# Performance work log

Measured on AMD Instinct MI355X. Metric: run time of the kernel, lower is better.

Reference implementation:

```python
import jax, jax.numpy as jnp
import numpy as np

N_NODES = 50000
NEG_SLOPE = 0.2


def _gat_conv(x, src, dst, W, a_src, a_dst, b, num_nodes):
    # W: [H*C, F_in]; a_src/a_dst: [H, C]; b: [H*C]
    H, C = a_src.shape
    xp = (x @ W.T).reshape(num_nodes, H, C)              # [N,H,C]
    alpha_s = jnp.sum(xp * a_src[None], axis=-1)          # [N,H]
    alpha_d = jnp.sum(xp * a_dst[None], axis=-1)          # [N,H]
    e = jax.nn.leaky_relu(alpha_s[src] + alpha_d[dst], NEG_SLOPE)  # [E,H]
    # segment softmax over incoming edges of each dst node (self-loops guarantee non-empty segments)
    m = jax.ops.segment_max(e, dst, num_segments=num_nodes)
    e = jnp.exp(e - m[dst])
    s = jax.ops.segment_sum(e, dst, num_segments=num_nodes)
    alpha = e / s[dst]                                    # [E,H]
    out = jax.ops.segment_sum(alpha[:, :, None] * xp[src], dst, num_segments=num_nodes)  # [N,H,C]
    return out.reshape(num_nodes, H * C) + b


def setup_inputs() -> dict:
    key = jax.random.key(0)
    ks = jax.random.split(key, 12)
    N, E, F_in, HID, H, Z = N_NODES, 800000, 128, 64, 2, 32
    sc = 0.1
    return {
        "features": jax.random.normal(ks[0], (N, F_in), jnp.float32),
        "edges": jax.random.randint(ks[1], (2, E), 0, N, jnp.int32),
        "W1": jax.random.normal(ks[2], (H * HID, F_in), jnp.float32) * sc,
        "a_src1": jax.random.normal(ks[3], (H, HID), jnp.float32) * sc,
        "a_dst1": jax.random.normal(ks[4], (H, HID), jnp.float32) * sc,
        "b1": jnp.zeros((H * HID,), jnp.float32),
        "W_mu": jax.random.normal(ks[5], (Z, H * HID), jnp.float32) * sc,
        "a_src_mu": jax.random.normal(ks[6], (1, Z), jnp.float32) * sc,
        "a_dst_mu": jax.random.normal(ks[7], (1, Z), jnp.float32) * sc,
        "b_mu": jnp.zeros((Z,), jnp.float32),
        "W_std": jax.random.normal(ks[8], (Z, H * HID), jnp.float32) * sc,
        "a_src_std": jax.random.normal(ks[9], (1, Z), jnp.float32) * sc,
        "a_dst_std": jax.random.normal(ks[10], (1, Z), jnp.float32) * sc,
        "b_std": jnp.zeros((Z,), jnp.float32),
    }


def reference(features, edges, W1, a_src1, a_dst1, b1, W_mu, a_src_mu, a_dst_mu, b_mu, W_std, a_src_std, a_dst_std, b_std):
    N = features.shape[0]
    loops = jnp.arange(N, dtype=edges.dtype)
    src = jnp.concatenate([edges[0], loops])  # add self loops (PyG default)
    dst = jnp.concatenate([edges[1], loops])
    h = _gat_conv(features, src, dst, W1, a_src1, a_dst1, b1, N)
    h = jax.nn.relu(h)  # dropout p=0.0 -> identity
    mu = _gat_conv(h, src, dst, W_mu, a_src_mu, a_dst_mu, b_mu, N)
    std = _gat_conv(h, src, dst, W_std, a_src_std, a_dst_std, b_std, N)
    return (mu, std)
```

## Files before the change

### kernel.cpp

```cpp
#include <hip/hip_runtime.h>
#include <math.h>

#define N_NODES 50000
#define N_EDGES 800000
#define ET (N_EDGES + N_NODES)
#define KD 128
#define Z 32
#define SH 7
#define BW 128
#define NBUCK ((N_NODES + BW - 1) / BW)
#define CHUNK 2048
#define NBLKA ((ET + CHUNK - 1) / CHUNK)
#define MTOT (NBUCK * NBLKA)
#define MBS ((MTOT + 1023) / 1024)

typedef __attribute__((ext_vector_type(8))) short bf16x8;
typedef __attribute__((ext_vector_type(4))) float f32x4;

static __device__ __forceinline__ float lrelu(float x){ return x > 0.f ? x : 0.2f*x; }
static __device__ __forceinline__ float bf2f(unsigned int u16){ return __uint_as_float(u16 << 16); }
static __device__ __forceinline__ unsigned short f2bf(float f){
  unsigned int x = __float_as_uint(f);
  return (unsigned short)((x + 0x7fffu + ((x >> 16) & 1u)) >> 16);
}

__global__ __launch_bounds__(256) void bhistA_kernel(const int* __restrict__ edges, int* __restrict__ M){
  int k = blockIdx.x, t = threadIdx.x;
  __shared__ int cnt[NBUCK];
  for(int b = t; b < NBUCK; b += 256) cnt[b] = 0;
  __syncthreads();
  int base = k*CHUNK;
  int lim = min(base + CHUNK, ET);
  for(int i = base + t; i < lim; i += 256){
    int d = (i < N_EDGES) ? edges[N_EDGES + i] : (i - N_EDGES);
    atomicAdd(&cnt[d >> SH], 1);
  }
  __syncthreads();
  for(int b = t; b < NBUCK; b += 256) M[b*NBLKA + k] = cnt[b];
}

__global__ __launch_bounds__(256) void scanM1_kernel(const int* __restrict__ M, int* __restrict__ bsumM){
  int b = blockIdx.x, t = threadIdx.x;
  int base = b*1024 + t*4;
  int s = 0;
  #pragma unroll
  for(int i=0;i<4;i++){ int n = base+i; if(n < MTOT) s += M[n]; }
  for(int off=32; off; off>>=1) s += __shfl_xor(s, off);
  __shared__ int ws[4];
  if((t&63)==0) ws[t>>6] = s;
  __syncthreads();
  if(t==0) bsumM[b] = ws[0]+ws[1]+ws[2]+ws[3];
}

__global__ __launch_bounds__(256) void scanM2_kernel(const int* __restrict__ bsumM, int* __restrict__ bpreM){
  __shared__ int sm[256];
  int t = threadIdx.x;
  int v = (t < MBS) ? bsumM[t] : 0;
  sm[t] = v;
  __syncthreads();
  for(int off=1; off<256; off<<=1){
    int u = (t >= off) ? sm[t-off] : 0;
    __syncthreads();
    sm[t] += u;
    __syncthreads();
  }
  if(t < MBS) bpreM[t] = sm[t] - v;
}

__global__ __launch_bounds__(256) void scanM3_kernel(const int* __restrict__ M, const int* __restrict__ bpreM,
                                                     int* __restrict__ Mpos){
  int b = blockIdx.x, t = threadIdx.x;
  int lane = t & 63, wv = t >> 6;
  int base = b*1024 + t*4;
  int d[4]; int s = 0;
  #pragma unroll
  for(int i=0;i<4;i++){ int n = base+i; d[i] = (n < MTOT) ? M[n] : 0; s += d[i]; }
  int v = s;
  for(int off=1; off<64; off<<=1){
    int u = __shfl_up(v, off);
    if(lane >= off) v += u;
  }
  int texcl = v - s;
  __shared__ int wtot[4];
  if(lane == 63) wtot[wv] = v;
  __syncthreads();
  int woff = 0;
  for(int i=0;i<wv;i++) woff += wtot[i];
  int run = bpreM[b] + woff + texcl;
  #pragma unroll
  for(int i=0;i<4;i++){
    int n = base+i;
    if(n < MTOT){ Mpos[n] = run; run += d[i]; }
  }
}

__global__ __launch_bounds__(256) void bplaceA_kernel(const int* __restrict__ edges, const int* __restrict__ Mpos,
                                                      int2* __restrict__ etmp){
  int k = blockIdx.x, t = threadIdx.x;
  __shared__ int cur[NBUCK];
  for(int b = t; b < NBUCK; b += 256) cur[b] = Mpos[b*NBLKA + k];
  __syncthreads();
  int base = k*CHUNK;
  int lim = min(base + CHUNK, ET);
  for(int i = base + t; i < lim; i += 256){
    int s, d;
    if(i < N_EDGES){ s = edges[i]; d = edges[N_EDGES+i]; } else { s = d = i - N_EDGES; }
    int pos = atomicAdd(&cur[d >> SH], 1);
    etmp[pos] = make_int2(s, d);
  }
}

__global__ __launch_bounds__(256) void bfin_kernel(const int* __restrict__ Mpos, const int2* __restrict__ etmp,
                                                   int* __restrict__ rowptr, int2* __restrict__ epair){
  int b = blockIdx.x, t = threadIdx.x;
  __shared__ int cnt[BW];
  __shared__ int pre[BW];
  __shared__ int lcur[BW];
  if(t < BW) cnt[t] = 0;
  __syncthreads();
  int beg = Mpos[b*NBLKA];
  int end = (b+1 < NBUCK) ? Mpos[(b+1)*NBLKA] : ET;
  for(int i = beg + t; i < end; i += 256) atomicAdd(&cnt[etmp[i].y & (BW-1)], 1);
  __syncthreads();
  if(t < BW) pre[t] = cnt[t];
  __syncthreads();
  for(int off=1; off<BW; off<<=1){
    int u = 0;
    if(t < BW && t >= off) u = pre[t-off];
    __syncthreads();
    if(t < BW) pre[t] += u;
    __syncthreads();
  }
  if(t < BW){
    int excl = pre[t] - cnt[t];
    int node = b*BW + t;
    if(node < N_NODES) rowptr[node] = beg + excl;
    lcur[t] = beg + excl;
  }
  if(b == 0 && t == 255) rowptr[N_NODES] = ET;
  __syncthreads();
  for(int i = beg + t; i < end; i += 256){
    int2 e = etmp[i];
    int pos = atomicAdd(&lcur[e.y & (BW-1)], 1);
    epair[pos] = e;
  }
}

__global__ __launch_bounds__(256) void wconv_kernel(const float* __restrict__ W1,
                                                    const float* __restrict__ Wmu, const float* __restrict__ Wst,
                                                    unsigned short* __restrict__ Wb1, unsigned short* __restrict__ Wb2){
  int i = blockIdx.x*256 + threadIdx.x;
  if(i < 128*KD) Wb1[i] = f2bf(W1[i]);
  if(i < 64*KD) Wb2[i] = f2bf(i < 32*KD ? Wmu[i] : Wst[i - 32*KD]);
}

__global__ __launch_bounds__(256) void mmt1_kernel(const float* __restrict__ X,
                                                   const unsigned short* __restrict__ Wb,
                                                   const float* __restrict__ asv, const float* __restrict__ adv,
                                                   unsigned short* __restrict__ outb,
                                                   float* __restrict__ as1, float* __restrict__ ad1){
  constexpr int OC = 128, CT = 8;
  int t = threadIdx.x;
  int w = t >> 6, L = t & 63;
  int col = L & 15, quad = L >> 4;
  int row0 = blockIdx.x*64 + w*16;
  int rA = row0 + col;
  if(rA >= N_NODES) rA = N_NODES-1;

  f32x4 acc[CT];
  #pragma unroll
  for(int ct=0;ct<CT;ct++) acc[ct] = (f32x4){0.f,0.f,0.f,0.f};

  #pragma unroll
  for(int kc=0;kc<4;kc++){
    int k0 = kc*32 + quad*8;
    const float* Xf = X + (size_t)rA*KD + k0;
    float4 p = *(const float4*)Xf;
    float4 q = *(const float4*)(Xf + 4);
    bf16x8 a;
    a[0] = (short)f2bf(p.x); a[1] = (short)f2bf(p.y);
    a[2] = (short)f2bf(p.z); a[3] = (short)f2bf(p.w);
    a[4] = (short)f2bf(q.x); a[5] = (short)f2bf(q.y);
    a[6] = (short)f2bf(q.z); a[7] = (short)f2bf(q.w);
    #pragma unroll
    for(int ct=0;ct<CT;ct++){
      bf16x8 b = *(const bf16x8*)(Wb + (size_t)(ct*16 + col)*KD + k0);
      acc[ct] = __builtin_amdgcn_mfma_f32_16x16x32_bf16(a, b, acc[ct], 0, 0, 0);
    }
  }

  float av[CT], dv[CT];
  #pragma unroll
  for(int ct=0;ct<CT;ct++){ av[ct] = asv[ct*16 + col]; dv[ct] = adv[ct*16 + col]; }

  #pragma unroll
  for(int r=0;r<4;r++){
    int row = row0 + quad*4 + r;
    #pragma unroll
    for(int ct=0;ct<CT;ct++)
      if(row < N_NODES) outb[(size_t)row*OC + ct*16 + col] = f2bf(acc[ct][r]);
    float s0 = acc[0][r]*av[0] + acc[1][r]*av[1] + acc[2][r]*av[2] + acc[3][r]*av[3];
    float s1 = acc[4][r]*av[4] + acc[5][r]*av[5] + acc[6][r]*av[6] + acc[7][r]*av[7];
    float d0 = acc[0][r]*dv[0] + acc[1][r]*dv[1] + acc[2][r]*dv[2] + acc[3][r]*dv[3];
    float d1 = acc[4][r]*dv[4] + acc[5][r]*dv[5] + acc[6][r]*dv[6] + acc[7][r]*dv[7];
    #pragma unroll
    for(int off=1; off<16; off<<=1){
      s0 += __shfl_xor(s0, off); s1 += __shfl_xor(s1, off);
      d0 += __shfl_xor(d0, off); d1 += __shfl_xor(d1, off);
    }
    if(col == 0 && row < N_NODES){
      as1[row*2] = s0; as1[row*2+1] = s1;
      ad1[row*2] = d0; ad1[row*2+1] = d1;
    }
  }
}

__global__ __launch_bounds__(256) void mmt2_kernel(const unsigned short* __restrict__ Xb,
                                                   const unsigned short* __restrict__ Wb,
                                                   const float* __restrict__ asmu, const float* __restrict__ admu,
                                                   const float* __restrict__ asst, const float* __restrict__ adst,
                                                   unsigned short* __restrict__ outb,
                                                   float* __restrict__ as2, float* __restrict__ ad2){
  constexpr int OC = 64, CT = 4;
  int t = threadIdx.x;
  int w = t >> 6, L = t & 63;
  int col = L & 15, quad = L >> 4;
  int row0 = blockIdx.x*64 + w*16;
  int rA = row0 + col;
  if(rA >= N_NODES) rA = N_NODES-1;

  f32x4 acc[CT];
  #pragma unroll
  for(int ct=0;ct<CT;ct++) acc[ct] = (f32x4){0.f,0.f,0.f,0.f};

  #pragma unroll
  for(int kc=0;kc<4;kc++){
    int k0 = kc*32 + quad*8;
    bf16x8 a = *(const bf16x8*)(Xb + (size_t)rA*KD + k0);
    #pragma unroll
    for(int ct=0;ct<CT;ct++){
      bf16x8 b = *(const bf16x8*)(Wb + (size_t)(ct*16 + col)*KD + k0);
      acc[ct] = __builtin_amdgcn_mfma_f32_16x16x32_bf16(a, b, acc[ct], 0, 0, 0);
    }
  }

  float av[CT], dv[CT];
  #pragma unroll
  for(int ct=0;ct<CT;ct++){
    av[ct] = (ct < 2) ? asmu[ct*16 + col] : asst[(ct-2)*16 + col];
    dv[ct] = (ct < 2) ? admu[ct*16 + col] : adst[(ct-2)*16 + col];
  }

  #pragma unroll
  for(int r=0;r<4;r++){
    int row = row0 + quad*4 + r;
    #pragma unroll
    for(int ct=0;ct<CT;ct++)
      if(row < N_NODES) outb[(size_t)row*OC + ct*16 + col] = f2bf(acc[ct][r]);
    float smu = acc[0][r]*av[0] + acc[1][r]*av[1];
    float sst = acc[2][r]*av[2] + acc[3][r]*av[3];
    float dmu = acc[0][r]*dv[0] + acc[1][r]*dv[1];
    float dst = acc[2][r]*dv[2] + acc[3][r]*dv[3];
    #pragma unroll
    for(int off=1; off<16; off<<=1){
      smu += __shfl_xor(smu, off); sst += __shfl_xor(sst, off);
      dmu += __shfl_xor(dmu, off); dst += __shfl_xor(dst, off);
    }
    if(col == 0 && row < N_NODES){
      as2[row*2] = smu; as2[row*2+1] = sst;
      ad2[row*2] = dmu; ad2[row*2+1] = dst;
    }
  }
}

__global__ __launch_bounds__(256) void wcalc_kernel(const int2* __restrict__ epair,
                                                    const float* __restrict__ asv, const float* __restrict__ adv,
                                                    float2* __restrict__ wbuf){
  int i = blockIdx.x*256 + threadIdx.x;
  if(i >= ET) return;
  int2 e = epair[i];
  float2 a = ((const float2*)asv)[e.x];
  float2 b = ((const float2*)adv)[e.y];
  float2 w;
  w.x = __expf(lrelu(a.x + b.x));
  w.y = __expf(lrelu(a.y + b.y));
  wbuf[i] = w;
}

__global__ __launch_bounds__(256) void agg1_kernel(const int* __restrict__ rowptr, const int2* __restrict__ epair,
                                                   const float2* __restrict__ wbuf, const unsigned int* __restrict__ xb,
                                                   const float* __restrict__ b1, unsigned int* __restrict__ hb){
  int node = blockIdx.x*4 + (threadIdx.x>>6);
  int l = threadIdx.x & 63;
  if(node >= N_NODES) return;
  int beg = rowptr[node], end = rowptr[node+1];
  float accx = 0.f, accy = 0.f, s0 = 0.f, s1 = 0.f;
  int n = end - beg;
  int nq = n & ~7;
  for(int q = 0; q < nq; q += 8){
    int e0 = epair[beg+q+0].x, e1 = epair[beg+q+1].x, e2 = epair[beg+q+2].x, e3 = epair[beg+q+3].x;
    int e4 = epair[beg+q+4].x, e5 = epair[beg+q+5].x, e6 = epair[beg+q+6].x, e7 = epair[beg+q+7].x;
    float2 w0 = wbuf[beg+q+0], w1 = wbuf[beg+q+1], w2 = wbuf[beg+q+2], w3 = wbuf[beg+q+3];
    float2 w4 = wbuf[beg+q+4], w5 = wbuf[beg+q+5], w6 = wbuf[beg+q+6], w7 = wbuf[beg+q+7];
    unsigned int u0 = xb[(size_t)e0*64 + l], u1 = xb[(size_t)e1*64 + l];
    unsigned int u2 = xb[(size_t)e2*64 + l], u3 = xb[(size_t)e3*64 + l];
    unsigned int u4 = xb[(size_t)e4*64 + l], u5 = xb[(size_t)e5*64 + l];
    unsigned int u6 = xb[(size_t)e6*64 + l], u7 = xb[(size_t)e7*64 + l];
    s0 += w0.x + w1.x + w2.x + w3.x + w4.x + w5.x + w6.x + w7.x;
    s1 += w0.y + w1.y + w2.y + w3.y + w4.y + w5.y + w6.y + w7.y;
    float v0 = (l < 32) ? w0.x : w0.y;
    float v1 = (l < 32) ? w1.x : w1.y;
    float v2 = (l < 32) ? w2.x : w2.y;
    float v3 = (l < 32) ? w3.x : w3.y;
    float v4 = (l < 32) ? w4.x : w4.y;
    float v5 = (l < 32) ? w5.x : w5.y;
    float v6 = (l < 32) ? w6.x : w6.y;
    float v7 = (l < 32) ? w7.x : w7.y;
    accx += v0*__uint_as_float(u0<<16) + v1*__uint_as_float(u1<<16)
          + v2*__uint_as_float(u2<<16) + v3*__uint_as_float(u3<<16)
          + v4*__uint_as_float(u4<<16) + v5*__uint_as_float(u5<<16)
          + v6*__uint_as_float(u6<<16) + v7*__uint_as_float(u7<<16);
    accy += v0*__uint_as_float(u0&0xffff0000u) + v1*__uint_as_float(u1&0xffff0000u)
          + v2*__uint_as_float(u2&0xffff0000u) + v3*__uint_as_float(u3&0xffff0000u)
          + v4*__uint_as_float(u4&0xffff0000u) + v5*__uint_as_float(u5&0xffff0000u)
          + v6*__uint_as_float(u6&0xffff0000u) + v7*__uint_as_float(u7&0xffff0000u);
  }
  for(int i = beg + nq; i < end; i++){
    int s = epair[i].x;
    float2 w = wbuf[i];
    s0 += w.x; s1 += w.y;
    unsigned int u = xb[(size_t)s*64 + l];
    float ww = (l < 32) ? w.x : w.y;
    accx += ww * __uint_as_float(u<<16);
    accy += ww * __uint_as_float(u&0xffff0000u);
  }
  float sd = (l < 32) ? s0 : s1;
  float2 bb = ((const float2*)b1)[l];
  float rx = fmaxf(accx/sd + bb.x, 0.f);
  float ry = fmaxf(accy/sd + bb.y, 0.f);
  unsigned int hp = (unsigned int)f2bf(rx) | ((unsigned int)f2bf(ry) << 16);
  hb[(size_t)node*64 + l] = hp;
}

__global__ __launch_bounds__(256) void agg2_kernel(const int* __restrict__ rowptr, const int2* __restrict__ epair,
                                                   const float2* __restrict__ wbuf, const unsigned short* __restrict__ xb2,
                                                   const float* __restrict__ bmu, const float* __restrict__ bst,
                                                   float* __restrict__ out){
  int node = blockIdx.x*4 + (threadIdx.x>>6);
  int l = threadIdx.x & 63;
  if(node >= N_NODES) return;
  int half = l >> 5, c = l & 31;
  int beg = rowptr[node], end = rowptr[node+1];
  float acc = 0.f, ssum = 0.f;
  int n = end - beg;
  int nq = n & ~7;
  for(int q = 0; q < nq; q += 8){
    int e0 = epair[beg+q+0].x, e1 = epair[beg+q+1].x, e2 = epair[beg+q+2].x, e3 = epair[beg+q+3].x;
    int e4 = epair[beg+q+4].x, e5 = epair[beg+q+5].x, e6 = epair[beg+q+6].x, e7 = epair[beg+q+7].x;
    float2 w0 = wbuf[beg+q+0], w1 = wbuf[beg+q+1], w2 = wbuf[beg+q+2], w3 = wbuf[beg+q+3];
    float2 w4 = wbuf[beg+q+4], w5 = wbuf[beg+q+5], w6 = wbuf[beg+q+6], w7 = wbuf[beg+q+7];
    float x0 = bf2f(xb2[(size_t)e0*64 + l]), x1 = bf2f(xb2[(size_t)e1*64 + l]);
    float x2 = bf2f(xb2[(size_t)e2*64 + l]), x3 = bf2f(xb2[(size_t)e3*64 + l]);
    float x4 = bf2f(xb2[(size_t)e4*64 + l]), x5 = bf2f(xb2[(size_t)e5*64 + l]);
    float x6 = bf2f(xb2[(size_t)e6*64 + l]), x7 = bf2f(xb2[(size_t)e7*64 + l]);
    float v0 = half ? w0.y : w0.x;
    float v1 = half ? w1.y : w1.x;
    float v2 = half ? w2.y : w2.x;
    float v3 = half ? w3.y : w3.x;
    float v4 = half ? w4.y : w4.x;
    float v5 = half ? w5.y : w5.x;
    float v6 = half ? w6.y : w6.x;
    float v7 = half ? w7.y : w7.x;
    ssum += v0 + v1 + v2 + v3 + v4 + v5 + v6 + v7;
    acc  += v0*x0 + v1*x1 + v2*x2 + v3*x3 + v4*x4 + v5*x5 + v6*x6 + v7*x7;
  }
  for(int i = beg + nq; i < end; i++){
    int s = epair[i].x;
    float2 w = wbuf[i];
    float ww = half ? w.y : w.x;
    ssum += ww;
    acc += ww * bf2f(xb2[(size_t)s*64 + l]);
  }
  float r = acc/ssum + (half ? bst[c] : bmu[c]);
  out[(half ? (size_t)N_NODES*Z : 0) + (size_t)node*Z + c] = r;
}

extern "C" void kernel_launch(void* const* d_in, const int* in_sizes, int n_in,
                              void* d_out, int out_size, void* d_ws, size_t ws_size,
                              hipStream_t stream){
  const float* x    = (const float*)d_in[0];
  const int*   edges= (const int*)d_in[1];
  const float* W1   = (const float*)d_in[2];
  const float* as1v = (const float*)d_in[3];
  const float* ad1v = (const float*)d_in[4];
  const float* b1   = (const float*)d_in[5];
  const float* Wmu  = (const float*)d_in[6];
  const float* asmu = (const float*)d_in[7];
  const float* admu = (const float*)d_in[8];
  const float* bmu  = (const float*)d_in[9];
  const float* Wst  = (const float*)d_in[10];
  const float* asst = (const float*)d_in[11];
  const float* adst = (const float*)d_in[12];
  const float* bst  = (const float*)d_in[13];
  float* out = (float*)d_out;

  char* p = (char*)d_ws;
  auto alloc = [&](size_t bytes)->char*{ char* r = p; p += (bytes + 255) & ~size_t(255); return r; };
  int*   M      = (int*)  alloc((size_t)MTOT*4);
  int*   Mpos   = (int*)  alloc((size_t)MTOT*4);
  int*   bsumM  = (int*)  alloc((size_t)MBS*4);
  int*   bpreM  = (int*)  alloc((size_t)MBS*4);
  int2*  etmp   = (int2*) alloc((size_t)ET*8);
  int2*  epair  = (int2*) alloc((size_t)ET*8);
  int*   rowptr = (int*)  alloc((size_t)(N_NODES+1)*4);
  unsigned short* Wb1 = (unsigned short*)alloc((size_t)128*KD*2);
  unsigned short* Wb2 = (unsigned short*)alloc((size_t)64*KD*2);
  unsigned short* xpb1 = (unsigned short*)alloc((size_t)N_NODES*128*2);
  float* as1    = (float*)alloc((size_t)N_NODES*2*4);
  float* ad1    = (float*)alloc((size_t)N_NODES*2*4);
  unsigned short* hb = (unsigned short*)alloc((size_t)N_NODES*128*2);
  float2* wbuf  = (float2*)alloc((size_t)ET*8);
  float* as2    = (float*)alloc((size_t)N_NODES*2*4);
  float* ad2    = (float*)alloc((size_t)N_NODES*2*4);
  unsigned short* xpb2 = xpb1;

  bhistA_kernel  <<<NBLKA, 256, 0, stream>>>(edges, M);
  scanM1_kernel  <<<MBS, 256, 0, stream>>>(M, bsumM);
  scanM2_kernel  <<<1, 256, 0, stream>>>(bsumM, bpreM);
  scanM3_kernel  <<<MBS, 256, 0, stream>>>(M, bpreM, Mpos);
  bplaceA_kernel <<<NBLKA, 256, 0, stream>>>(edges, Mpos, etmp);
  bfin_kernel    <<<NBUCK, 256, 0, stream>>>(Mpos, etmp, rowptr, epair);

  wconv_kernel   <<<(128*KD + 255)/256, 256, 0, stream>>>(W1, Wmu, Wst, Wb1, Wb2);

  mmt1_kernel <<<(N_NODES+63)/64, 256, 0, stream>>>(x, Wb1, as1v, ad1v, xpb1, as1, ad1);
  wcalc_kernel<<<(ET+255)/256, 256, 0, stream>>>(epair, as1, ad1, wbuf);
  agg1_kernel <<<(N_NODES+3)/4, 256, 0, stream>>>(rowptr, epair, wbuf, (const unsigned int*)xpb1, b1, (unsigned int*)hb);

  mmt2_kernel <<<(N_NODES+63)/64, 256, 0, stream>>>(hb, Wb2, asmu, admu, asst, adst, xpb1, as2, ad2);
  wcalc_kernel<<<(ET+255)/256, 256, 0, stream>>>(epair, as2, ad2, wbuf);
  agg2_kernel <<<(N_NODES+3)/4, 256, 0, stream>>>(rowptr, epair, wbuf, xpb2, bmu, bst, out);
}
```

Baseline: 262.1 us.

## Split wavefront across edges with wider per-lane loads in aggregation kernels

Both aggregation kernels now split each wavefront into sub-groups that process different edges at once. Each lane loads 8 bytes (four bf16 features) instead of 2–4 bytes, and partial sums are combined with cross-lane shuffles at the end. This is meant to raise memory-level parallelism and cut per-edge instruction overhead on the gather-bound neighbor aggregation. The cost is extra shuffle reductions, idle lanes during the final store, and uneven work when a node's edge count is not a multiple of the group count.

```diff
diff --git a/kernel.cpp b/kernel.cpp
--- a/kernel.cpp
+++ b/kernel.cpp
@@ -19,6 +19,8 @@
 
 static __device__ __forceinline__ float lrelu(float x){ return x > 0.f ? x : 0.2f*x; }
 static __device__ __forceinline__ float bf2f(unsigned int u16){ return __uint_as_float(u16 << 16); }
+static __device__ __forceinline__ float lof(unsigned int u){ return __uint_as_float(u << 16); }
+static __device__ __forceinline__ float hif(unsigned int u){ return __uint_as_float(u & 0xffff0000u); }
 static __device__ __forceinline__ unsigned short f2bf(float f){
   unsigned int x = __float_as_uint(f);
   return (unsigned short)((x + 0x7fffu + ((x >> 16) & 1u)) >> 16);
@@ -288,101 +290,128 @@
 }
 
 __global__ __launch_bounds__(256) void agg1_kernel(const int* __restrict__ rowptr, const int2* __restrict__ epair,
-                                                   const float2* __restrict__ wbuf, const unsigned int* __restrict__ xb,
-                                                   const float* __restrict__ b1, unsigned int* __restrict__ hb){
+                                                   const float2* __restrict__ wbuf, const uint2* __restrict__ xb,
+                                                   const float* __restrict__ b1, uint2* __restrict__ hb){
   int node = blockIdx.x*4 + (threadIdx.x>>6);
   int l = threadIdx.x & 63;
   if(node >= N_NODES) return;
+  int half = l >> 5, c = l & 31;
   int beg = rowptr[node], end = rowptr[node+1];
-  float accx = 0.f, accy = 0.f, s0 = 0.f, s1 = 0.f;
   int n = end - beg;
-  int nq = n & ~7;
-  for(int q = 0; q < nq; q += 8){
-    int e0 = epair[beg+q+0].x, e1 = epair[beg+q+1].x, e2 = epair[beg+q+2].x, e3 = epair[beg+q+3].x;
-    int e4 = epair[beg+q+4].x, e5 = epair[beg+q+5].x, e6 = epair[beg+q+6].x, e7 = epair[beg+q+7].x;
-    float2 w0 = wbuf[beg+q+0], w1 = wbuf[beg+q+1], w2 = wbuf[beg+q+2], w3 = wbuf[beg+q+3];
-    float2 w4 = wbuf[beg+q+4], w5 = wbuf[beg+q+5], w6 = wbuf[beg+q+6], w7 = wbuf[beg+q+7];
-    unsigned int u0 = xb[(size_t)e0*64 + l], u1 = xb[(size_t)e1*64 + l];
-    unsigned int u2 = xb[(size_t)e2*64 + l], u3 = xb[(size_t)e3*64 + l];
-    unsigned int u4 = xb[(size_t)e4*64 + l], u5 = xb[(size_t)e5*64 + l];
-    unsigned int u6 = xb[(size_t)e6*64 + l], u7 = xb[(size_t)e7*64 + l];
-    s0 += w0.x + w1.x + w2.x + w3.x + w4.x + w5.x + w6.x + w7.x;
-    s1 += w0.y + w1.y + w2.y + w3.y + w4.y + w5.y + w6.y + w7.y;
-    float v0 = (l < 32) ? w0.x : w0.y;
-    float v1 = (l < 32) ? w1.x : w1.y;
-    float v2 = (l < 32) ? w2.x : w2.y;
-    float v3 = (l < 32) ? w3.x : w3.y;
-    float v4 = (l < 32) ? w4.x : w4.y;
-    float v5 = (l < 32) ? w5.x : w5.y;
-    float v6 = (l < 32) ? w6.x : w6.y;
-    float v7 = (l < 32) ? w7.x : w7.y;
-    accx += v0*__uint_as_float(u0<<16) + v1*__uint_as_float(u1<<16)
-          + v2*__uint_as_float(u2<<16) + v3*__uint_as_float(u3<<16)
-          + v4*__uint_as_float(u4<<16) + v5*__uint_as_float(u5<<16)
-          + v6*__uint_as_float(u6<<16) + v7*__uint_as_float(u7<<16);
-    accy += v0*__uint_as_float(u0&0xffff0000u) + v1*__uint_as_float(u1&0xffff0000u)
-          + v2*__uint_as_float(u2&0xffff0000u) + v3*__uint_as_float(u3&0xffff0000u)
-          + v4*__uint_as_float(u4&0xffff0000u) + v5*__uint_as_float(u5&0xffff0000u)
-          + v6*__uint_as_float(u6&0xffff0000u) + v7*__uint_as_float(u7&0xffff0000u);
-  }
-  for(int i = beg + nq; i < end; i++){
-    int s = epair[i].x;
-    float2 w = wbuf[i];
+  float a0=0.f, a1=0.f, a2=0.f, a3=0.f, s0=0.f, s1=0.f;
+  int npair = n >> 1;
+  int mainp = npair & ~7;
+
+#define G1(j) int e##j = epair[base + 2*j].x; float2 w##j = wbuf[base + 2*j];
+#define U1(j) uint2 u##j = xb[(size_t)e##j*32 + c];
+#define C1(j) { s0 += w##j.x; s1 += w##j.y; \
+                float vv = (c < 16) ? w##j.x : w##j.y; \
+                a0 += vv*lof(u##j.x); a1 += vv*hif(u##j.x); \
+                a2 += vv*lof(u##j.y); a3 += vv*hif(u##j.y); }
+
+  for(int pq = 0; pq < mainp; pq += 8){
+    int base = beg + 2*pq + half;
+    G1(0) G1(1) G1(2) G1(3) G1(4) G1(5) G1(6) G1(7)
+    U1(0) U1(1) U1(2) U1(3) U1(4) U1(5) U1(6) U1(7)
+    C1(0) C1(1) C1(2) C1(3) C1(4) C1(5) C1(6) C1(7)
+  }
+  for(int pq = mainp; pq < npair; pq++){
+    int base = beg + 2*pq + half;
+    G1(0) U1(0) C1(0)
+  }
+  if((n & 1) && half == 0){
+    int idx = beg + n - 1;
+    int e = epair[idx].x;
+    float2 w = wbuf[idx];
+    uint2 u = xb[(size_t)e*32 + c];
     s0 += w.x; s1 += w.y;
-    unsigned int u = xb[(size_t)s*64 + l];
-    float ww = (l < 32) ? w.x : w.y;
-    accx += ww * __uint_as_float(u<<16);
-    accy += ww * __uint_as_float(u&0xffff0000u);
-  }
-  float sd = (l < 32) ? s0 : s1;
-  float2 bb = ((const float2*)b1)[l];
-  float rx = fmaxf(accx/sd + bb.x, 0.f);
-  float ry = fmaxf(accy/sd + bb.y, 0.f);
-  unsigned int hp = (unsigned int)f2bf(rx) | ((unsigned int)f2bf(ry) << 16);
-  hb[(size_t)node*64 + l] = hp;
+    float vv = (c < 16) ? w.x : w.y;
+    a0 += vv*lof(u.x); a1 += vv*hif(u.x);
+    a2 += vv*lof(u.y); a3 += vv*hif(u.y);
+  }
+#undef G1
+#undef U1
+#undef C1
+  s0 += __shfl_xor(s0, 32); s1 += __shfl_xor(s1, 32);
+  a0 += __shfl_xor(a0, 32); a1 += __shfl_xor(a1, 32);
+  a2 += __shfl_xor(a2, 32); a3 += __shfl_xor(a3, 32);
+  float sd = (c < 16) ? s0 : s1;
+  float4 bb = *(const float4*)(b1 + 4*c);
+  float r0 = fmaxf(a0/sd + bb.x, 0.f);
+  float r1 = fmaxf(a1/sd + bb.y, 0.f);
+  float r2 = fmaxf(a2/sd + bb.z, 0.f);
+  float r3 = fmaxf(a3/sd + bb.w, 0.f);
+  if(half == 0){
+    uint2 o;
+    o.x = (unsigned)f2bf(r0) | ((unsigned)f2bf(r1) << 16);
+    o.y = (unsigned)f2bf(r2) | ((unsigned)f2bf(r3) << 16);
+    hb[(size_t)node*32 + c] = o;
+  }
 }
 
 __global__ __launch_bounds__(256) void agg2_kernel(const int* __restrict__ rowptr, const int2* __restrict__ epair,
-                                                   const float2* __restrict__ wbuf, const unsigned short* __restrict__ xb2,
+                                                   const float2* __restrict__ wbuf, const uint2* __restrict__ xb2,
                                                    const float* __restrict__ bmu, const float* __restrict__ bst,
                                                    float* __restrict__ out){
   int node = blockIdx.x*4 + (threadIdx.x>>6);
   int l = threadIdx.x & 63;
   if(node >= N_NODES) return;
-  int half = l >> 5, c = l & 31;
+  int g = l >> 4, c = l & 15;
   int beg = rowptr[node], end = rowptr[node+1];
-  float acc = 0.f, ssum = 0.f;
   int n = end - beg;
-  int nq = n & ~7;
-  for(int q = 0; q < nq; q += 8){
-    int e0 = epair[beg+q+0].x, e1 = epair[beg+q+1].x, e2 = epair[beg+q+2].x, e3 = epair[beg+q+3].x;
-    int e4 = epair[beg+q+4].x, e5 = epair[beg+q+5].x, e6 = epair[beg+q+6].x, e7 = epair[beg+q+7].x;
-    float2 w0 = wbuf[beg+q+0], w1 = wbuf[beg+q+1], w2 = wbuf[beg+q+2], w3 = wbuf[beg+q+3];
-    float2 w4 = wbuf[beg+q+4], w5 = wbuf[beg+q+5], w6 = wbuf[beg+q+6], w7 = wbuf[beg+q+7];
-    float x0 = bf2f(xb2[(size_t)e0*64 + l]), x1 = bf2f(xb2[(size_t)e1*64 + l]);
-    float x2 = bf2f(xb2[(size_t)e2*64 + l]), x3 = bf2f(xb2[(size_t)e3*64 + l]);
-    float x4 = bf2f(xb2[(size_t)e4*64 + l]), x5 = bf2f(xb2[(size_t)e5*64 + l]);
-    float x6 = bf2f(xb2[(size_t)e6*64 + l]), x7 = bf2f(xb2[(size_t)e7*64 + l]);
-    float v0 = half ? w0.y : w0.x;
-    float v1 = half ? w1.y : w1.x;
-    float v2 = half ? w2.y : w2.x;
-    float v3 = half ? w3.y : w3.x;
-    float v4 = half ? w4.y : w4.x;
-    float v5 = half ? w5.y : w5.x;
-    float v6 = half ? w6.y : w6.x;
-    float v7 = half ? w7.y : w7.x;
-    ssum += v0 + v1 + v2 + v3 + v4 + v5 + v6 + v7;
-    acc  += v0*x0 + v1*x1 + v2*x2 + v3*x3 + v4*x4 + v5*x5 + v6*x6 + v7*x7;
-  }
-  for(int i = beg + nq; i < end; i++){
-    int s = epair[i].x;
-    float2 w = wbuf[i];
-    float ww = half ? w.y : w.x;
-    ssum += ww;
-    acc += ww * bf2f(xb2[(size_t)s*64 + l]);
-  }
-  float r = acc/ssum + (half ? bst[c] : bmu[c]);
-  out[(half ? (size_t)N_NODES*Z : 0) + (size_t)node*Z + c] = r;
+  float a0=0.f, a1=0.f, a2=0.f, a3=0.f, smu=0.f, sst=0.f;
+  int nquad = n >> 2;
+  int mainq = nquad & ~3;
+
+#define G2(j) int e##j = epair[base + 4*j].x; float2 w##j = wbuf[base + 4*j];
+#define U2(j) uint2 u##j = xb2[(size_t)e##j*16 + c];
+#define C2(j) { smu += w##j.x; sst += w##j.y; \
+                float vv = (c < 8) ? w##j.x : w##j.y; \
+                a0 += vv*lof(u##j.x); a1 += vv*hif(u##j.x); \
+                a2 += vv*lof(u##j.y); a3 += vv*hif(u##j.y); }
+
+  for(int qq = 0; qq < mainq; qq += 4){
+    int base = beg + 4*qq + g;
+    G2(0) G2(1) G2(2) G2(3)
+    U2(0) U2(1) U2(2) U2(3)
+    C2(0) C2(1) C2(2) C2(3)
+  }
+  for(int qq = mainq; qq < nquad; qq++){
+    int base = beg + 4*qq + g;
+    G2(0) U2(0) C2(0)
+  }
+  int tail = n & 3;
+  if(g < tail){
+    int idx = beg + 4*nquad + g;
+    int e = epair[idx].x;
+    float2 w = wbuf[idx];
+    uint2 u = xb2[(size_t)e*16 + c];
+    smu += w.x; sst += w.y;
+    float vv = (c < 8) ? w.x : w.y;
+    a0 += vv*lof(u.x); a1 += vv*hif(u.x);
+    a2 += vv*lof(u.y); a3 += vv*hif(u.y);
+  }
+#undef G2
+#undef U2
+#undef C2
+  #pragma unroll
+  for(int off = 16; off < 64; off <<= 1){
+    smu += __shfl_xor(smu, off); sst += __shfl_xor(sst, off);
+    a0 += __shfl_xor(a0, off); a1 += __shfl_xor(a1, off);
+    a2 += __shfl_xor(a2, off); a3 += __shfl_xor(a3, off);
+  }
+  float sd = (c < 8) ? smu : sst;
+  float4 bb = (c < 8) ? *(const float4*)(bmu + 4*c) : *(const float4*)(bst + 4*(c-8));
+  float4 r;
+  r.x = a0/sd + bb.x;
+  r.y = a1/sd + bb.y;
+  r.z = a2/sd + bb.z;
+  r.w = a3/sd + bb.w;
+  if(g == 0){
+    float* dst = (c < 8) ? (out + (size_t)node*Z + 4*c)
+                         : (out + (size_t)N_NODES*Z + (size_t)node*Z + 4*(c-8));
+    *(float4*)dst = r;
+  }
 }
 
 extern "C" void kernel_launch(void* const* d_in, const int* in_sizes, int n_in,
@@ -435,9 +464,9 @@
 
   mmt1_kernel <<<(N_NODES+63)/64, 256, 0, stream>>>(x, Wb1, as1v, ad1v, xpb1, as1, ad1);
   wcalc_kernel<<<(ET+255)/256, 256, 0, stream>>>(epair, as1, ad1, wbuf);
-  agg1_kernel <<<(N_NODES+3)/4, 256, 0, stream>>>(rowptr, epair, wbuf, (const unsigned int*)xpb1, b1, (unsigned int*)hb);
+  agg1_kernel <<<(N_NODES+3)/4, 256, 0, stream>>>(rowptr, epair, wbuf, (const uint2*)xpb1, b1, (uint2*)hb);
 
   mmt2_kernel <<<(N_NODES+63)/64, 256, 0, stream>>>(hb, Wb2, asmu, admu, asst, adst, xpb1, as2, ad2);
   wcalc_kernel<<<(ET+255)/256, 256, 0, stream>>>(epair, as2, ad2, wbuf);
-  agg2_kernel <<<(N_NODES+3)/4, 256, 0, stream>>>(rowptr, epair, wbuf, xpb2, bmu, bst, out);
-}
+  agg2_kernel <<<(N_NODES+3)/4, 256, 0, stream>>>(rowptr, epair, wbuf, (const uint2*)xpb2, bmu, bst, out);
+}
```

After: 250.5 us. -4.4%, faster.
